# Optimization experiments

Hardware: AMD Instinct MI355X
Metric: run time of the kernel (lower is better)

## Reference

```python
import jax, jax.numpy as jnp
import numpy as np

N, E, IN_DIM, HIDDEN, OUT_DIM = 100000, 800000, 128, 128, 40
EPS = 1e-5


def setup_inputs() -> dict:
    key = jax.random.key(0)
    ks = jax.random.split(key, 20)
    x = jax.random.normal(ks[0], (N, IN_DIM), dtype=jnp.float32)
    edge_index = jax.random.randint(ks[1], (2, E), 0, N, dtype=jnp.int64)

    def lin(k, fan_in, fan_out):
        return jax.random.normal(k, (fan_in, fan_out), dtype=jnp.float32) / np.sqrt(fan_in)

    d = {"x": x, "edge_index": edge_index}
    dims = [(IN_DIM, HIDDEN), (HIDDEN, HIDDEN), (HIDDEN, HIDDEN), (HIDDEN, OUT_DIM)]
    ki = 2
    for i, (fi, fo) in enumerate(dims, start=1):
        d[f"Wl{i}"] = lin(ks[ki], fi, fo); ki += 1   # lin_l: applied to aggregated neighbors (has bias)
        d[f"bl{i}"] = jnp.zeros((fo,), jnp.float32)
        d[f"Wr{i}"] = lin(ks[ki], fi, fo); ki += 1   # lin_r: applied to root node (no bias, PyG default)
    for i in (1, 2, 3):
        d[f"g{i}"] = jnp.ones((HIDDEN,), jnp.float32)   # BatchNorm gamma
        d[f"b{i}"] = jnp.zeros((HIDDEN,), jnp.float32)  # BatchNorm beta
    return d


def _sage_conv(x, src, dst, inv_cnt, Wl, bl, Wr):
    # mean-aggregate neighbor features: gather x[src], scatter-add at dst, divide by in-degree
    agg = jax.ops.segment_sum(x[src], dst, num_segments=N) * inv_cnt  # [N, F]
    return agg @ Wl + bl + x @ Wr


def _bn(x, g, b):
    # batch-statistics normalization (training-mode BatchNorm1d, biased variance)
    mu = jnp.mean(x, axis=0)
    var = jnp.mean(jnp.square(x - mu), axis=0)
    return (x - mu) * jax.lax.rsqrt(var + EPS) * g + b


def reference(x, edge_index, Wl1, bl1, Wr1, Wl2, bl2, Wr2, Wl3, bl3, Wr3,
              Wl4, bl4, Wr4, g1, b1, g2, b2, g3, b3):
    src, dst = edge_index[0], edge_index[1]
    cnt = jax.ops.segment_sum(jnp.ones((E,), jnp.float32), dst, num_segments=N)
    inv_cnt = (1.0 / jnp.maximum(cnt, 1.0))[:, None]  # [N, 1]

    h = jax.nn.relu(_bn(_sage_conv(x, src, dst, inv_cnt, Wl1, bl1, Wr1), g1, b1))
    h = jax.nn.relu(_bn(_sage_conv(h, src, dst, inv_cnt, Wl2, bl2, Wr2), g2, b2))
    h = jax.nn.relu(_bn(_sage_conv(h, src, dst, inv_cnt, Wl3, bl3, Wr3), g3, b3))
    out = _sage_conv(h, src, dst, inv_cnt, Wl4, bl4, Wr4)
    return jax.nn.log_softmax(out, axis=1)
```

## Files before the change

### kernel.cpp

```cpp
#include <hip/hip_runtime.h>
#include <math.h>

#define NN 100000
#define NE 800000
#define F 128
#define KK 256
#define OUTD 40
#define EPSF 1e-5f
#define NB 391
#define FROWS 32

__global__ void detect_kernel(const int* __restrict__ ei_raw, int* __restrict__ flag) {
  __shared__ int any;
  if (threadIdx.x == 0) any = 0;
  __syncthreads();
  if (ei_raw[2 * threadIdx.x + 1] != 0) atomicOr(&any, 1);
  __syncthreads();
  if (threadIdx.x == 0) *flag = (any == 0) ? 1 : 0;
}

__global__ __launch_bounds__(256) void conv_kernel(const int* __restrict__ ei_raw,
                                                   const int* __restrict__ flag,
                                                   int* __restrict__ es) {
  int i = blockIdx.x * 256 + threadIdx.x;
  if (i < 2 * NE) {
    int f = *flag;
    es[i] = f ? ei_raw[2 * i] : ei_raw[i];
  }
}

__global__ __launch_bounds__(256) void deg_kernel(const int* __restrict__ dst,
                                                  int* __restrict__ deg) {
  int e = blockIdx.x * 256 + threadIdx.x;
  if (e < NE) atomicAdd(&deg[dst[e]], 1);
}

__global__ __launch_bounds__(256) void scan1(const int* __restrict__ deg,
                                             int* __restrict__ offs,
                                             int* __restrict__ bsum) {
  __shared__ int sh[256];
  const int tid = threadIdx.x;
  const int i = blockIdx.x * 256 + tid;
  int v = (i < NN) ? deg[i] : 0;
  sh[tid] = v;
  __syncthreads();
#pragma unroll
  for (int off = 1; off < 256; off <<= 1) {
    int add = (tid >= off) ? sh[tid - off] : 0;
    __syncthreads();
    sh[tid] += add;
    __syncthreads();
  }
  if (i < NN) offs[i] = sh[tid] - v;
  if (tid == 255) bsum[blockIdx.x] = sh[255];
}

__global__ void scan2(int* __restrict__ bsum) {
  __shared__ int sh[512];
  const int t = threadIdx.x;
  int v = (t < NB) ? bsum[t] : 0;
  sh[t] = v;
  __syncthreads();
#pragma unroll
  for (int off = 1; off < 512; off <<= 1) {
    int add = (t >= off) ? sh[t - off] : 0;
    __syncthreads();
    sh[t] += add;
    __syncthreads();
  }
  if (t < NB) bsum[t] = sh[t] - v;
}

__global__ __launch_bounds__(256) void scan3(int* __restrict__ offs,
                                             int* __restrict__ woff,
                                             const int* __restrict__ bsum) {
  int i = blockIdx.x * 256 + threadIdx.x;
  if (i < NN) {
    int o = offs[i] + bsum[blockIdx.x];
    offs[i] = o;
    woff[i] = o;
  }
  if (i == 0) offs[NN] = NE;
}

__global__ __launch_bounds__(256) void fill_kernel(const int* __restrict__ src,
                                                   const int* __restrict__ dst,
                                                   int* __restrict__ woff,
                                                   int* __restrict__ eidx) {
  int e = blockIdx.x * 256 + threadIdx.x;
  if (e < NE) {
    int pos = atomicAdd(&woff[dst[e]], 1);
    eidx[pos] = src[e];
  }
}

__global__ __launch_bounds__(256) void transpose_w(const float* __restrict__ Wl,
                                                   const float* __restrict__ Wr,
                                                   float* __restrict__ Wt) {
  int i = blockIdx.x * 256 + threadIdx.x;
  if (i < OUTD * KK) {
    int j = i / KK, k = i - j * KK;
    Wt[i] = (k < F) ? Wl[k * OUTD + j] : Wr[(k - F) * OUTD + j];
  }
}

template <int BN>
__global__ __launch_bounds__(256) void gather_kernel(const float* __restrict__ xin,
                                                     const int* __restrict__ eidx,
                                                     const int* __restrict__ offs,
                                                     const float* __restrict__ sc,
                                                     float* __restrict__ agg) {
  int tid = blockIdx.x * 256 + threadIdx.x;
  int n = tid >> 5;
  int q = tid & 31;
  int beg = offs[n];
  int end = offs[n + 1];
  float4 scl, shf;
  if (BN) {
    scl = *(const float4*)(sc + q * 4);
    shf = *(const float4*)(sc + 128 + q * 4);
  }
  float ax = 0.f, ay = 0.f, az = 0.f, aw = 0.f;
#define ACCV(vv)                                         \
  do {                                                   \
    if (BN) {                                            \
      vv.x = fmaxf(fmaf(vv.x, scl.x, shf.x), 0.f);       \
      vv.y = fmaxf(fmaf(vv.y, scl.y, shf.y), 0.f);       \
      vv.z = fmaxf(fmaf(vv.z, scl.z, shf.z), 0.f);       \
      vv.w = fmaxf(fmaf(vv.w, scl.w, shf.w), 0.f);       \
    }                                                    \
    ax += vv.x; ay += vv.y; az += vv.z; aw += vv.w;      \
  } while (0)
  int i = beg;
  for (; i + 8 <= end; i += 8) {
    int s0 = eidx[i],     s1 = eidx[i + 1], s2 = eidx[i + 2], s3 = eidx[i + 3];
    int s4 = eidx[i + 4], s5 = eidx[i + 5], s6 = eidx[i + 6], s7 = eidx[i + 7];
    float4 v0 = *(const float4*)(xin + (size_t)s0 * F + q * 4);
    float4 v1 = *(const float4*)(xin + (size_t)s1 * F + q * 4);
    float4 v2 = *(const float4*)(xin + (size_t)s2 * F + q * 4);
    float4 v3 = *(const float4*)(xin + (size_t)s3 * F + q * 4);
    float4 v4 = *(const float4*)(xin + (size_t)s4 * F + q * 4);
    float4 v5 = *(const float4*)(xin + (size_t)s5 * F + q * 4);
    float4 v6 = *(const float4*)(xin + (size_t)s6 * F + q * 4);
    float4 v7 = *(const float4*)(xin + (size_t)s7 * F + q * 4);
    ACCV(v0); ACCV(v1); ACCV(v2); ACCV(v3);
    ACCV(v4); ACCV(v5); ACCV(v6); ACCV(v7);
  }
  for (; i + 2 <= end; i += 2) {
    int s0 = eidx[i], s1 = eidx[i + 1];
    float4 v0 = *(const float4*)(xin + (size_t)s0 * F + q * 4);
    float4 v1 = *(const float4*)(xin + (size_t)s1 * F + q * 4);
    ACCV(v0); ACCV(v1);
  }
  if (i < end) {
    int s0 = eidx[i];
    float4 v0 = *(const float4*)(xin + (size_t)s0 * F + q * 4);
    ACCV(v0);
  }
#undef ACCV
  float m = 1.0f / fmaxf((float)(end - beg), 1.0f);
  float4 o;
  o.x = ax * m; o.y = ay * m; o.z = az * m; o.w = aw * m;
  *(float4*)(agg + (size_t)n * F + q * 4) = o;
}

template <int BN>
__global__ __launch_bounds__(256) void gemm_fused(const float* __restrict__ agg,
                                                  const float* __restrict__ xin,
                                                  const float* __restrict__ sc,
                                                  const float* __restrict__ Wl,
                                                  const float* __restrict__ bl,
                                                  const float* __restrict__ Wr,
                                                  float* __restrict__ out,
                                                  float* __restrict__ sums) {
  __shared__ float tile[32][KK];
  const int t = threadIdx.x;
  const int row0 = blockIdx.x * 32;
#pragma unroll
  for (int i = 0; i < 8; ++i) {
    int slot = t + i * 256;
    int r = slot >> 6;
    int c4 = slot & 63;
    int row = row0 + r;
    float4 v;
    if (c4 < 32) {
      v = *(const float4*)(agg + (size_t)row * F + c4 * 4);
    } else {
      int c = (c4 - 32) * 4;
      v = *(const float4*)(xin + (size_t)row * F + c);
      if (BN) {
        float4 s4 = *(const float4*)(sc + c);
        float4 b4 = *(const float4*)(sc + 128 + c);
        v.x = fmaxf(fmaf(v.x, s4.x, b4.x), 0.f);
        v.y = fmaxf(fmaf(v.y, s4.y, b4.y), 0.f);
        v.z = fmaxf(fmaf(v.z, s4.z, b4.z), 0.f);
        v.w = fmaxf(fmaf(v.w, s4.w, b4.w), 0.f);
      }
    }
    *(float4*)(&tile[r][c4 * 4]) = v;
  }
  __syncthreads();

  const int tx = t & 31;
  const int ty = t >> 5;
  float acc[4][4];
#pragma unroll
  for (int r = 0; r < 4; ++r)
#pragma unroll
    for (int c = 0; c < 4; ++c) acc[r][c] = 0.f;

#pragma unroll 1
  for (int half = 0; half < 2; ++half) {
    const float* __restrict__ Wp = half ? Wr : Wl;
    const int kb = half * 128;
    for (int k = 0; k < 128; k += 4) {
      float4 in4[4];
#pragma unroll
      for (int r = 0; r < 4; ++r)
        in4[r] = *(const float4*)(&tile[ty * 4 + r][kb + k]);
#pragma unroll
      for (int i = 0; i < 4; ++i) {
        float4 w = *(const float4*)(Wp + (size_t)(k + i) * F + tx * 4);
        float a[4];
        a[0] = ((const float*)&in4[0])[i];
        a[1] = ((const float*)&in4[1])[i];
        a[2] = ((const float*)&in4[2])[i];
        a[3] = ((const float*)&in4[3])[i];
#pragma unroll
        for (int r = 0; r < 4; ++r) {
          acc[r][0] = fmaf(a[r], w.x, acc[r][0]);
          acc[r][1] = fmaf(a[r], w.y, acc[r][1]);
          acc[r][2] = fmaf(a[r], w.z, acc[r][2]);
          acc[r][3] = fmaf(a[r], w.w, acc[r][3]);
        }
      }
    }
  }
  float4 b4 = *(const float4*)(bl + tx * 4);
  float ps[4] = {0.f, 0.f, 0.f, 0.f};
  float pq[4] = {0.f, 0.f, 0.f, 0.f};
#pragma unroll
  for (int r = 0; r < 4; ++r) {
    float4 o;
    o.x = acc[r][0] + b4.x;
    o.y = acc[r][1] + b4.y;
    o.z = acc[r][2] + b4.z;
    o.w = acc[r][3] + b4.w;
    ps[0] += o.x; pq[0] = fmaf(o.x, o.x, pq[0]);
    ps[1] += o.y; pq[1] = fmaf(o.y, o.y, pq[1]);
    ps[2] += o.z; pq[2] = fmaf(o.z, o.z, pq[2]);
    ps[3] += o.w; pq[3] = fmaf(o.w, o.w, pq[3]);
    *(float4*)(out + (size_t)(row0 + ty * 4 + r) * F + tx * 4) = o;
  }
  __syncthreads();
  float* red = &tile[0][0];
#pragma unroll
  for (int j = 0; j < 4; ++j) {
    red[ty * 128 + tx * 4 + j] = ps[j];
    red[2048 + ty * 128 + tx * 4 + j] = pq[j];
  }
  __syncthreads();
  if (t < 128) {
    float s = 0.f, qq = 0.f;
#pragma unroll
    for (int g2 = 0; g2 < 8; ++g2) {
      s += red[g2 * 128 + t];
      qq += red[2048 + g2 * 128 + t];
    }
    atomicAdd(&sums[t], s);
    atomicAdd(&sums[128 + t], qq);
  }
}

__global__ void bn_params(const float* __restrict__ sums, const float* __restrict__ g,
                          const float* __restrict__ b, float* __restrict__ sc) {
  int c = threadIdx.x;
  float mu = sums[c] * (1.0f / NN);
  float var = sums[128 + c] * (1.0f / NN) - mu * mu;
  float scale = g[c] * rsqrtf(var + EPSF);
  sc[c] = scale;
  sc[128 + c] = b[c] - mu * scale;
}

__global__ __launch_bounds__(256) void final_kernel(const float* __restrict__ agg,
                                                    const float* __restrict__ h,
                                                    const float* __restrict__ sc,
                                                    const float* __restrict__ Wt,
                                                    const float* __restrict__ bl,
                                                    float* __restrict__ out) {
  __shared__ float tile[FROWS][KK];
  const int t = threadIdx.x;
  const int row0 = blockIdx.x * FROWS;
#pragma unroll
  for (int i = 0; i < 8; ++i) {
    int slot = t + i * 256;
    int r = slot >> 6, c4 = slot & 63;
    int row = row0 + r;
    float4 v;
    if (c4 < 32) {
      v = *(const float4*)(agg + (size_t)row * F + c4 * 4);
    } else {
      int c = (c4 - 32) * 4;
      v = *(const float4*)(h + (size_t)row * F + c);
      float4 s4 = *(const float4*)(sc + c);
      float4 b4 = *(const float4*)(sc + 128 + c);
      v.x = fmaxf(fmaf(v.x, s4.x, b4.x), 0.f);
      v.y = fmaxf(fmaf(v.y, s4.y, b4.y), 0.f);
      v.z = fmaxf(fmaf(v.z, s4.z, b4.z), 0.f);
      v.w = fmaxf(fmaf(v.w, s4.w, b4.w), 0.f);
    }
    *(float4*)(&tile[r][c4 * 4]) = v;
  }
  __syncthreads();
  const int tx = t & 63;
  const int wv = t >> 6;
  const int jj = (tx < OUTD) ? tx : 0;
  const float* __restrict__ wrow = Wt + (size_t)jj * KK;
  float acc[8] = {0.f, 0.f, 0.f, 0.f, 0.f, 0.f, 0.f, 0.f};
#pragma unroll 2
  for (int k = 0; k < KK; k += 4) {
    float4 w = *(const float4*)(wrow + k);
#pragma unroll
    for (int r = 0; r < 8; ++r) {
      float4 a = *(const float4*)(&tile[wv * 8 + r][k]);
      acc[r] = fmaf(a.x, w.x, acc[r]);
      acc[r] = fmaf(a.y, w.y, acc[r]);
      acc[r] = fmaf(a.z, w.z, acc[r]);
      acc[r] = fmaf(a.w, w.w, acc[r]);
    }
  }
  float bias = bl[jj];
#pragma unroll
  for (int r = 0; r < 8; ++r) {
    float v = acc[r] + bias;
    float m = (tx < OUTD) ? v : -INFINITY;
#pragma unroll
    for (int off = 32; off > 0; off >>= 1) m = fmaxf(m, __shfl_xor(m, off));
    float e = (tx < OUTD) ? expf(v - m) : 0.f;
    float s = e;
#pragma unroll
    for (int off = 32; off > 0; off >>= 1) s += __shfl_xor(s, off);
    if (tx < OUTD) out[(size_t)(row0 + wv * 8 + r) * OUTD + tx] = v - m - logf(s);
  }
}

extern "C" void kernel_launch(void* const* d_in, const int* in_sizes, int n_in,
                              void* d_out, int out_size, void* d_ws, size_t ws_size,
                              hipStream_t stream) {
  const float* x = (const float*)d_in[0];
  const int* ei_raw = (const int*)d_in[1];
  const float* Wl[4] = {(const float*)d_in[2], (const float*)d_in[5],
                        (const float*)d_in[8], (const float*)d_in[11]};
  const float* bl[4] = {(const float*)d_in[3], (const float*)d_in[6],
                        (const float*)d_in[9], (const float*)d_in[12]};
  const float* Wr[4] = {(const float*)d_in[4], (const float*)d_in[7],
                        (const float*)d_in[10], (const float*)d_in[13]};
  const float* g[3] = {(const float*)d_in[14], (const float*)d_in[16],
                       (const float*)d_in[18]};
  const float* bb[3] = {(const float*)d_in[15], (const float*)d_in[17],
                        (const float*)d_in[19]};

  char* wsb = (char*)d_ws;
  float* agg = (float*)wsb;                       wsb += (size_t)NN * F * 4;
  float* hA  = (float*)wsb;                       wsb += (size_t)NN * F * 4;
  float* hB  = (float*)wsb;                       wsb += (size_t)NN * F * 4;
  int* es    = (int*)wsb;                         wsb += (size_t)2 * NE * 4;
  int* eidx  = (int*)wsb;                         wsb += (size_t)NE * 4;
  int* offs  = (int*)wsb;                         wsb += (size_t)(NN + 64) * 4;
  int* woff  = (int*)wsb;                         wsb += (size_t)(NN + 64) * 4;
  int* bsum  = (int*)wsb;                         wsb += 512 * 4;
  float* sums = (float*)wsb;                      wsb += 256 * 4;
  float* sc   = (float*)wsb;                      wsb += 256 * 4;
  float* Wt   = (float*)wsb;                      wsb += (size_t)OUTD * KK * 4;
  int* flag   = (int*)wsb;                        wsb += 256;

  int* esrc = es;
  int* edst = es + NE;

  detect_kernel<<<1, 256, 0, stream>>>(ei_raw, flag);
  conv_kernel<<<(2 * NE + 255) / 256, 256, 0, stream>>>(ei_raw, flag, es);

  hipMemsetAsync(woff, 0, NN * sizeof(int), stream);
  deg_kernel<<<NE / 256, 256, 0, stream>>>(edst, woff);
  scan1<<<NB, 256, 0, stream>>>(woff, offs, bsum);
  scan2<<<1, 512, 0, stream>>>(bsum);
  scan3<<<NB, 256, 0, stream>>>(offs, woff, bsum);
  fill_kernel<<<NE / 256, 256, 0, stream>>>(esrc, edst, woff, eidx);
  transpose_w<<<(OUTD * KK + 255) / 256, 256, 0, stream>>>(Wl[3], Wr[3], Wt);

  const float* cur = x;
  float* bufs[2] = {hA, hB};
  for (int L = 0; L < 3; ++L) {
    float* hpre = bufs[L & 1];
    if (L == 0)
      gather_kernel<0><<<NN * 32 / 256, 256, 0, stream>>>(cur, eidx, offs, nullptr, agg);
    else
      gather_kernel<1><<<NN * 32 / 256, 256, 0, stream>>>(cur, eidx, offs, sc, agg);
    hipMemsetAsync(sums, 0, 256 * sizeof(float), stream);
    if (L == 0)
      gemm_fused<0><<<NN / 32, 256, 0, stream>>>(agg, cur, nullptr, Wl[L], bl[L], Wr[L],
                                                 hpre, sums);
    else
      gemm_fused<1><<<NN / 32, 256, 0, stream>>>(agg, cur, sc, Wl[L], bl[L], Wr[L],
                                                 hpre, sums);
    bn_params<<<1, 128, 0, stream>>>(sums, g[L], bb[L], sc);
    cur = hpre;
  }
  gather_kernel<1><<<NN * 32 / 256, 256, 0, stream>>>(cur, eidx, offs, sc, agg);
  final_kernel<<<NN / FROWS, 256, 0, stream>>>(agg, cur, sc, Wt, bl[3],
                                               (float*)d_out);
}
```

Baseline: 990.6 us.

## Fuse neighbor gather into GEMM layer kernels, drop agg buffer

Merges the separate mean-aggregation gather kernel into the per-layer GEMM kernel and the final classifier kernel. Each block gathers neighbor means for its 32 rows into shared memory, runs the Wl half, then reloads the root rows into the same tile and runs the Wr half. This removes the write and reread of the N×128 agg buffer and four kernel launches. In exchange each block now serializes an irregular gather before its compute, unroll depth drops from 8 to 4, and each row's gather runs on a single warp, which may lower memory-level parallelism and cause load imbalance.

```diff
diff --git a/kernel.cpp b/kernel.cpp
--- a/kernel.cpp
+++ b/kernel.cpp
@@ -8,7 +8,6 @@
 #define OUTD 40
 #define EPSF 1e-5f
 #define NB 391
-#define FROWS 32
 
 __global__ void detect_kernel(const int* __restrict__ ei_raw, int* __restrict__ flag) {
   __shared__ int any;
@@ -104,101 +103,117 @@
   }
 }
 
+__device__ __forceinline__ void bnrelu4(float4& v, const float4& s, const float4& b) {
+  v.x = fmaxf(fmaf(v.x, s.x, b.x), 0.f);
+  v.y = fmaxf(fmaf(v.y, s.y, b.y), 0.f);
+  v.z = fmaxf(fmaf(v.z, s.z, b.z), 0.f);
+  v.w = fmaxf(fmaf(v.w, s.w, b.w), 0.f);
+}
+
 template <int BN>
-__global__ __launch_bounds__(256) void gather_kernel(const float* __restrict__ xin,
-                                                     const int* __restrict__ eidx,
-                                                     const int* __restrict__ offs,
-                                                     const float* __restrict__ sc,
-                                                     float* __restrict__ agg) {
-  int tid = blockIdx.x * 256 + threadIdx.x;
-  int n = tid >> 5;
-  int q = tid & 31;
-  int beg = offs[n];
-  int end = offs[n + 1];
+__device__ __forceinline__ void gather_phase(float (*tile)[F],
+                                             const float* __restrict__ hin,
+                                             const int* __restrict__ eidx,
+                                             const int* __restrict__ offs,
+                                             int row0, int q, int grp,
+                                             const float4& scl, const float4& shf) {
+#pragma unroll 1
+  for (int rr = 0; rr < 4; ++rr) {
+    int r = grp * 4 + rr;
+    int n = row0 + r;
+    int beg = offs[n];
+    int end = offs[n + 1];
+    float ax = 0.f, ay = 0.f, az = 0.f, aw = 0.f;
+#define ACCV(vv)                                       \
+  do {                                                 \
+    if (BN) bnrelu4(vv, scl, shf);                     \
+    ax += vv.x; ay += vv.y; az += vv.z; aw += vv.w;    \
+  } while (0)
+    int i = beg;
+    for (; i + 4 <= end; i += 4) {
+      int s0 = eidx[i], s1 = eidx[i + 1], s2 = eidx[i + 2], s3 = eidx[i + 3];
+      float4 v0 = *(const float4*)(hin + (size_t)s0 * F + q * 4);
+      float4 v1 = *(const float4*)(hin + (size_t)s1 * F + q * 4);
+      float4 v2 = *(const float4*)(hin + (size_t)s2 * F + q * 4);
+      float4 v3 = *(const float4*)(hin + (size_t)s3 * F + q * 4);
+      ACCV(v0); ACCV(v1); ACCV(v2); ACCV(v3);
+    }
+    for (; i < end; ++i) {
+      int s0 = eidx[i];
+      float4 v0 = *(const float4*)(hin + (size_t)s0 * F + q * 4);
+      ACCV(v0);
+    }
+#undef ACCV
+    float m = 1.0f / fmaxf((float)(end - beg), 1.0f);
+    float4 o;
+    o.x = ax * m; o.y = ay * m; o.z = az * m; o.w = aw * m;
+    *(float4*)(&tile[r][q * 4]) = o;
+  }
+}
+
+template <int BN>
+__device__ __forceinline__ void root_phase(float (*tile)[F],
+                                           const float* __restrict__ hin,
+                                           int row0, int q, int grp,
+                                           const float4& scl, const float4& shf) {
+#pragma unroll
+  for (int rr = 0; rr < 4; ++rr) {
+    int r = grp * 4 + rr;
+    float4 v = *(const float4*)(hin + (size_t)(row0 + r) * F + q * 4);
+    if (BN) bnrelu4(v, scl, shf);
+    *(float4*)(&tile[r][q * 4]) = v;
+  }
+}
+
+__device__ __forceinline__ void fma_half(const float (*tile)[F],
+                                         const float* __restrict__ Wp,
+                                         int tx, int ty, float acc[4][4]) {
+  for (int k = 0; k < F; k += 4) {
+    float4 in4[4];
+#pragma unroll
+    for (int r = 0; r < 4; ++r)
+      in4[r] = *(const float4*)(&tile[ty * 4 + r][k]);
+#pragma unroll
+    for (int i = 0; i < 4; ++i) {
+      float4 w = *(const float4*)(Wp + (size_t)(k + i) * F + tx * 4);
+      float a[4];
+      a[0] = ((const float*)&in4[0])[i];
+      a[1] = ((const float*)&in4[1])[i];
+      a[2] = ((const float*)&in4[2])[i];
+      a[3] = ((const float*)&in4[3])[i];
+#pragma unroll
+      for (int r = 0; r < 4; ++r) {
+        acc[r][0] = fmaf(a[r], w.x, acc[r][0]);
+        acc[r][1] = fmaf(a[r], w.y, acc[r][1]);
+        acc[r][2] = fmaf(a[r], w.z, acc[r][2]);
+        acc[r][3] = fmaf(a[r], w.w, acc[r][3]);
+      }
+    }
+  }
+}
+
+template <int BN>
+__global__ __launch_bounds__(256) void fused_layer(const float* __restrict__ hin,
+                                                   const int* __restrict__ eidx,
+                                                   const int* __restrict__ offs,
+                                                   const float* __restrict__ sc,
+                                                   const float* __restrict__ Wl,
+                                                   const float* __restrict__ bl,
+                                                   const float* __restrict__ Wr,
+                                                   float* __restrict__ out,
+                                                   float* __restrict__ sums) {
+  __shared__ float tile[32][F];
+  const int t = threadIdx.x;
+  const int row0 = blockIdx.x * 32;
+  const int q = t & 31;
+  const int grp = t >> 5;
   float4 scl, shf;
   if (BN) {
     scl = *(const float4*)(sc + q * 4);
     shf = *(const float4*)(sc + 128 + q * 4);
   }
-  float ax = 0.f, ay = 0.f, az = 0.f, aw = 0.f;
-#define ACCV(vv)                                         \
-  do {                                                   \
-    if (BN) {                                            \
-      vv.x = fmaxf(fmaf(vv.x, scl.x, shf.x), 0.f);       \
-      vv.y = fmaxf(fmaf(vv.y, scl.y, shf.y), 0.f);       \
-      vv.z = fmaxf(fmaf(vv.z, scl.z, shf.z), 0.f);       \
-      vv.w = fmaxf(fmaf(vv.w, scl.w, shf.w), 0.f);       \
-    }                                                    \
-    ax += vv.x; ay += vv.y; az += vv.z; aw += vv.w;      \
-  } while (0)
-  int i = beg;
-  for (; i + 8 <= end; i += 8) {
-    int s0 = eidx[i],     s1 = eidx[i + 1], s2 = eidx[i + 2], s3 = eidx[i + 3];
-    int s4 = eidx[i + 4], s5 = eidx[i + 5], s6 = eidx[i + 6], s7 = eidx[i + 7];
-    float4 v0 = *(const float4*)(xin + (size_t)s0 * F + q * 4);
-    float4 v1 = *(const float4*)(xin + (size_t)s1 * F + q * 4);
-    float4 v2 = *(const float4*)(xin + (size_t)s2 * F + q * 4);
-    float4 v3 = *(const float4*)(xin + (size_t)s3 * F + q * 4);
-    float4 v4 = *(const float4*)(xin + (size_t)s4 * F + q * 4);
-    float4 v5 = *(const float4*)(xin + (size_t)s5 * F + q * 4);
-    float4 v6 = *(const float4*)(xin + (size_t)s6 * F + q * 4);
-    float4 v7 = *(const float4*)(xin + (size_t)s7 * F + q * 4);
-    ACCV(v0); ACCV(v1); ACCV(v2); ACCV(v3);
-    ACCV(v4); ACCV(v5); ACCV(v6); ACCV(v7);
-  }
-  for (; i + 2 <= end; i += 2) {
-    int s0 = eidx[i], s1 = eidx[i + 1];
-    float4 v0 = *(const float4*)(xin + (size_t)s0 * F + q * 4);
-    float4 v1 = *(const float4*)(xin + (size_t)s1 * F + q * 4);
-    ACCV(v0); ACCV(v1);
-  }
-  if (i < end) {
-    int s0 = eidx[i];
-    float4 v0 = *(const float4*)(xin + (size_t)s0 * F + q * 4);
-    ACCV(v0);
-  }
-#undef ACCV
-  float m = 1.0f / fmaxf((float)(end - beg), 1.0f);
-  float4 o;
-  o.x = ax * m; o.y = ay * m; o.z = az * m; o.w = aw * m;
-  *(float4*)(agg + (size_t)n * F + q * 4) = o;
-}
-
-template <int BN>
-__global__ __launch_bounds__(256) void gemm_fused(const float* __restrict__ agg,
-                                                  const float* __restrict__ xin,
-                                                  const float* __restrict__ sc,
-                                                  const float* __restrict__ Wl,
-                                                  const float* __restrict__ bl,
-                                                  const float* __restrict__ Wr,
-                                                  float* __restrict__ out,
-                                                  float* __restrict__ sums) {
-  __shared__ float tile[32][KK];
-  const int t = threadIdx.x;
-  const int row0 = blockIdx.x * 32;
-#pragma unroll
-  for (int i = 0; i < 8; ++i) {
-    int slot = t + i * 256;
-    int r = slot >> 6;
-    int c4 = slot & 63;
-    int row = row0 + r;
-    float4 v;
-    if (c4 < 32) {
-      v = *(const float4*)(agg + (size_t)row * F + c4 * 4);
-    } else {
-      int c = (c4 - 32) * 4;
-      v = *(const float4*)(xin + (size_t)row * F + c);
-      if (BN) {
-        float4 s4 = *(const float4*)(sc + c);
-        float4 b4 = *(const float4*)(sc + 128 + c);
-        v.x = fmaxf(fmaf(v.x, s4.x, b4.x), 0.f);
-        v.y = fmaxf(fmaf(v.y, s4.y, b4.y), 0.f);
-        v.z = fmaxf(fmaf(v.z, s4.z, b4.z), 0.f);
-        v.w = fmaxf(fmaf(v.w, s4.w, b4.w), 0.f);
-      }
-    }
-    *(float4*)(&tile[r][c4 * 4]) = v;
-  }
+
+  gather_phase<BN>(tile, hin, eidx, offs, row0, q, grp, scl, shf);
   __syncthreads();
 
   const int tx = t & 31;
@@ -209,33 +224,14 @@
 #pragma unroll
     for (int c = 0; c < 4; ++c) acc[r][c] = 0.f;
 
-#pragma unroll 1
-  for (int half = 0; half < 2; ++half) {
-    const float* __restrict__ Wp = half ? Wr : Wl;
-    const int kb = half * 128;
-    for (int k = 0; k < 128; k += 4) {
-      float4 in4[4];
-#pragma unroll
-      for (int r = 0; r < 4; ++r)
-        in4[r] = *(const float4*)(&tile[ty * 4 + r][kb + k]);
-#pragma unroll
-      for (int i = 0; i < 4; ++i) {
-        float4 w = *(const float4*)(Wp + (size_t)(k + i) * F + tx * 4);
-        float a[4];
-        a[0] = ((const float*)&in4[0])[i];
-        a[1] = ((const float*)&in4[1])[i];
-        a[2] = ((const float*)&in4[2])[i];
-        a[3] = ((const float*)&in4[3])[i];
-#pragma unroll
-        for (int r = 0; r < 4; ++r) {
-          acc[r][0] = fmaf(a[r], w.x, acc[r][0]);
-          acc[r][1] = fmaf(a[r], w.y, acc[r][1]);
-          acc[r][2] = fmaf(a[r], w.z, acc[r][2]);
-          acc[r][3] = fmaf(a[r], w.w, acc[r][3]);
-        }
-      }
-    }
-  }
+  fma_half(tile, Wl, tx, ty, acc);
+  __syncthreads();
+
+  root_phase<BN>(tile, hin, row0, q, grp, scl, shf);
+  __syncthreads();
+
+  fma_half(tile, Wr, tx, ty, acc);
+
   float4 b4 = *(const float4*)(bl + tx * 4);
   float ps[4] = {0.f, 0.f, 0.f, 0.f};
   float pq[4] = {0.f, 0.f, 0.f, 0.f};
@@ -282,43 +278,31 @@
   sc[128 + c] = b[c] - mu * scale;
 }
 
-__global__ __launch_bounds__(256) void final_kernel(const float* __restrict__ agg,
-                                                    const float* __restrict__ h,
-                                                    const float* __restrict__ sc,
-                                                    const float* __restrict__ Wt,
-                                                    const float* __restrict__ bl,
-                                                    float* __restrict__ out) {
-  __shared__ float tile[FROWS][KK];
+__global__ __launch_bounds__(256) void fused_final(const float* __restrict__ hin,
+                                                   const int* __restrict__ eidx,
+                                                   const int* __restrict__ offs,
+                                                   const float* __restrict__ sc,
+                                                   const float* __restrict__ Wt,
+                                                   const float* __restrict__ bl,
+                                                   float* __restrict__ out) {
+  __shared__ float tile[32][F];
   const int t = threadIdx.x;
-  const int row0 = blockIdx.x * FROWS;
-#pragma unroll
-  for (int i = 0; i < 8; ++i) {
-    int slot = t + i * 256;
-    int r = slot >> 6, c4 = slot & 63;
-    int row = row0 + r;
-    float4 v;
-    if (c4 < 32) {
-      v = *(const float4*)(agg + (size_t)row * F + c4 * 4);
-    } else {
-      int c = (c4 - 32) * 4;
-      v = *(const float4*)(h + (size_t)row * F + c);
-      float4 s4 = *(const float4*)(sc + c);
-      float4 b4 = *(const float4*)(sc + 128 + c);
-      v.x = fmaxf(fmaf(v.x, s4.x, b4.x), 0.f);
-      v.y = fmaxf(fmaf(v.y, s4.y, b4.y), 0.f);
-      v.z = fmaxf(fmaf(v.z, s4.z, b4.z), 0.f);
-      v.w = fmaxf(fmaf(v.w, s4.w, b4.w), 0.f);
-    }
-    *(float4*)(&tile[r][c4 * 4]) = v;
-  }
-  __syncthreads();
+  const int row0 = blockIdx.x * 32;
+  const int q = t & 31;
+  const int grp = t >> 5;
+  float4 scl = *(const float4*)(sc + q * 4);
+  float4 shf = *(const float4*)(sc + 128 + q * 4);
+
+  gather_phase<1>(tile, hin, eidx, offs, row0, q, grp, scl, shf);
+  __syncthreads();
+
   const int tx = t & 63;
   const int wv = t >> 6;
   const int jj = (tx < OUTD) ? tx : 0;
   const float* __restrict__ wrow = Wt + (size_t)jj * KK;
   float acc[8] = {0.f, 0.f, 0.f, 0.f, 0.f, 0.f, 0.f, 0.f};
 #pragma unroll 2
-  for (int k = 0; k < KK; k += 4) {
+  for (int k = 0; k < F; k += 4) {
     float4 w = *(const float4*)(wrow + k);
 #pragma unroll
     for (int r = 0; r < 8; ++r) {
@@ -329,6 +313,24 @@
       acc[r] = fmaf(a.w, w.w, acc[r]);
     }
   }
+  __syncthreads();
+
+  root_phase<1>(tile, hin, row0, q, grp, scl, shf);
+  __syncthreads();
+
+#pragma unroll 2
+  for (int k = 0; k < F; k += 4) {
+    float4 w = *(const float4*)(wrow + F + k);
+#pragma unroll
+    for (int r = 0; r < 8; ++r) {
+      float4 a = *(const float4*)(&tile[wv * 8 + r][k]);
+      acc[r] = fmaf(a.x, w.x, acc[r]);
+      acc[r] = fmaf(a.y, w.y, acc[r]);
+      acc[r] = fmaf(a.z, w.z, acc[r]);
+      acc[r] = fmaf(a.w, w.w, acc[r]);
+    }
+  }
+
   float bias = bl[jj];
 #pragma unroll
   for (int r = 0; r < 8; ++r) {
@@ -361,7 +363,6 @@
                         (const float*)d_in[19]};
 
   char* wsb = (char*)d_ws;
-  float* agg = (float*)wsb;                       wsb += (size_t)NN * F * 4;
   float* hA  = (float*)wsb;                       wsb += (size_t)NN * F * 4;
   float* hB  = (float*)wsb;                       wsb += (size_t)NN * F * 4;
   int* es    = (int*)wsb;                         wsb += (size_t)2 * NE * 4;
@@ -392,21 +393,16 @@
   float* bufs[2] = {hA, hB};
   for (int L = 0; L < 3; ++L) {
     float* hpre = bufs[L & 1];
-    if (L == 0)
-      gather_kernel<0><<<NN * 32 / 256, 256, 0, stream>>>(cur, eidx, offs, nullptr, agg);
-    else
-      gather_kernel<1><<<NN * 32 / 256, 256, 0, stream>>>(cur, eidx, offs, sc, agg);
     hipMemsetAsync(sums, 0, 256 * sizeof(float), stream);
     if (L == 0)
-      gemm_fused<0><<<NN / 32, 256, 0, stream>>>(agg, cur, nullptr, Wl[L], bl[L], Wr[L],
-                                                 hpre, sums);
+      fused_layer<0><<<NN / 32, 256, 0, stream>>>(cur, eidx, offs, nullptr, Wl[L],
+                                                  bl[L], Wr[L], hpre, sums);
     else
-      gemm_fused<1><<<NN / 32, 256, 0, stream>>>(agg, cur, sc, Wl[L], bl[L], Wr[L],
-                                                 hpre, sums);
+      fused_layer<1><<<NN / 32, 256, 0, stream>>>(cur, eidx, offs, sc, Wl[L], bl[L],
+                                                  Wr[L], hpre, sums);
     bn_params<<<1, 128, 0, stream>>>(sums, g[L], bb[L], sc);
     cur = hpre;
   }
-  gather_kernel<1><<<NN * 32 / 256, 256, 0, stream>>>(cur, eidx, offs, sc, agg);
-  final_kernel<<<NN / FROWS, 256, 0, stream>>>(agg, cur, sc, Wt, bl[3],
-                                               (float*)d_out);
-}
+  fused_final<<<NN / 32, 256, 0, stream>>>(cur, eidx, offs, sc, Wt, bl[3],
+                                           (float*)d_out);
+}
```

New measurement: 875.0 us. -11.7%, faster.
